# Optimization experiments

Measured on AMD Instinct MI355X. Metric: run time of the kernel, lower is better.

Reference implementation:

```python
import jax, jax.numpy as jnp
import numpy as np

# static multi-scale pyramid (must match spatial_shapes array in setup_inputs)
SPATIAL = ((100, 100), (50, 50), (25, 25), (13, 13))
E, H, L, P = 256, 8, 4, 8   # embed_dims, num_heads, num_levels, num_points
BS, NQ = 2, 10000
LEN_VAL = sum(h * w for h, w in SPATIAL)


def _bilinear_gather(val, grid, Hs, Ws):
    """val: [BH, Hs*Ws, d]; grid: [BH, N, 2] in [-1,1].
    Matches F.grid_sample(mode='bilinear', padding_mode='zeros', align_corners=False)."""
    x = (grid[..., 0] + 1.0) * (Ws * 0.5) - 0.5
    y = (grid[..., 1] + 1.0) * (Hs * 0.5) - 0.5
    x0 = jnp.floor(x).astype(jnp.int32)
    y0 = jnp.floor(y).astype(jnp.int32)
    x1, y1 = x0 + 1, y0 + 1
    wx1 = x - x0.astype(x.dtype)
    wy1 = y - y0.astype(y.dtype)
    wx0, wy0 = 1.0 - wx1, 1.0 - wy1

    def corner(xi, yi, w):
        valid = (xi >= 0) & (xi < Ws) & (yi >= 0) & (yi < Hs)
        idx = jnp.clip(yi, 0, Hs - 1) * Ws + jnp.clip(xi, 0, Ws - 1)  # [BH, N]
        v = jnp.take_along_axis(val, idx[..., None], axis=1)          # [BH, N, d]
        return v * (w * valid.astype(w.dtype))[..., None]

    return (corner(x0, y0, wx0 * wy0) + corner(x1, y0, wx1 * wy0)
            + corner(x0, y1, wx0 * wy1) + corner(x1, y1, wx1 * wy1))


def setup_inputs() -> dict:
    key = jax.random.key(0)
    ks = jax.random.split(key, 10)
    scale = 1.0 / np.sqrt(E)
    inp = {
        'query': jax.random.normal(ks[0], (BS, NQ, E), jnp.float32),
        'value': jax.random.normal(ks[1], (BS, LEN_VAL, E), jnp.float32),
        'query_pos': 0.1 * jax.random.normal(ks[2], (BS, NQ, E), jnp.float32),
        'reference_points': jax.random.uniform(ks[3], (BS, NQ, L, 2), jnp.float32),
        'spatial_shapes': jnp.array(SPATIAL, dtype=jnp.int32),
        'W_off': 0.02 * jax.random.normal(ks[4], (E, H * L * P * 2), jnp.float32),
        'b_off': 0.5 * jax.random.normal(ks[5], (H * L * P * 2,), jnp.float32),
        'W_attn': 0.02 * jax.random.normal(ks[6], (E, H * L * P), jnp.float32),
        'b_attn': jnp.zeros((H * L * P,), jnp.float32),
        'W_val': scale * jax.random.normal(ks[7], (E, E), jnp.float32),
        'b_val': jnp.zeros((E,), jnp.float32),
        'W_out': scale * jax.random.normal(ks[8], (E, E), jnp.float32),
        'b_out': jnp.zeros((E,), jnp.float32),
    }
    return inp


def reference(query, value, query_pos, reference_points, spatial_shapes,
              W_off, b_off, W_attn, b_attn, W_val, b_val, W_out, b_out):
    d = E // H
    q = query + query_pos                                        # [bs, nq, E]
    bs, nq, _ = q.shape
    v = (value @ W_val + b_val).reshape(bs, LEN_VAL, H, d)       # [bs, len, H, d]
    off = (q @ W_off + b_off).reshape(bs, nq, H, L, P, 2)
    aw = jax.nn.softmax((q @ W_attn + b_attn).reshape(bs, nq, H, L * P), axis=-1)
    aw = aw.reshape(bs, nq, H, L, P)
    # normalizer is (W, H) per level
    norm = jnp.stack([spatial_shapes[:, 1], spatial_shapes[:, 0]], -1).astype(q.dtype)
    loc = reference_points[:, :, None, :, None, :] + off / norm[None, None, None, :, None, :]
    grids = 2.0 * loc - 1.0                                      # [bs, nq, H, L, P, 2]

    out = jnp.zeros((bs, nq, H, d), q.dtype)
    start = 0
    for lvl, (Hs, Ws) in enumerate(SPATIAL):
        v_l = v[:, start:start + Hs * Ws]                        # [bs, HW, H, d]
        start += Hs * Ws
        v_l = v_l.transpose(0, 2, 1, 3).reshape(bs * H, Hs * Ws, d)
        g_l = grids[:, :, :, lvl].transpose(0, 2, 1, 3, 4).reshape(bs * H, nq * P, 2)
        s = _bilinear_gather(v_l, g_l, Hs, Ws).reshape(bs, H, nq, P, d)
        w_l = aw[:, :, :, lvl].transpose(0, 2, 1, 3)             # [bs, H, nq, P]
        out = out + jnp.einsum('bhnpc,bhnp->bnhc', s, w_l)
    return out.reshape(bs, nq, E) @ W_out + b_out
```

## Files before the change

kernel.cpp:

```cpp
#include <hip/hip_runtime.h>


#define EE   256
#define HH   8
#define LL   4
#define NQq  10000
#define BSB  2
#define LENV 13294
#define MQ   16
#define ROWS_V (BSB * LENV)

#define VWS_OFF 393216

typedef unsigned short u16;
typedef unsigned int   u32;
typedef __attribute__((ext_vector_type(8))) short bf16x8;
typedef __attribute__((ext_vector_type(4))) float f32x4;

__device__ __forceinline__ u32 bf16_of(float f) {
  u32 u = __float_as_uint(f);
  return (u + 0x7FFFu + ((u >> 16) & 1u)) >> 16;
}
__device__ __forceinline__ float blo(u32 u) { return __uint_as_float(u << 16); }
__device__ __forceinline__ float bhi(u32 u) { return __uint_as_float(u & 0xFFFF0000u); }

__device__ __forceinline__ uint4 pack8(const float* f) {
  uint4 u;
  u.x = bf16_of(f[0]) | (bf16_of(f[1]) << 16);
  u.y = bf16_of(f[2]) | (bf16_of(f[3]) << 16);
  u.z = bf16_of(f[4]) | (bf16_of(f[5]) << 16);
  u.w = bf16_of(f[6]) | (bf16_of(f[7]) << 16);
  return u;
}

__device__ __forceinline__ void acc8(float o[8], uint4 q, float w) {
  o[0] += w * blo(q.x); o[1] += w * bhi(q.x);
  o[2] += w * blo(q.y); o[3] += w * bhi(q.y);
  o[4] += w * blo(q.z); o[5] += w * bhi(q.z);
  o[6] += w * blo(q.w); o[7] += w * bhi(q.w);
}

__global__ __launch_bounds__(64) void k_prep(
    const float* __restrict__ W_off, const float* __restrict__ W_attn,
    const float* __restrict__ W_val, const float* __restrict__ W_out,
    u16* __restrict__ wcat, u16* __restrict__ wval, u16* __restrict__ wout) {
  const int tile = blockIdx.x >> 3, s = blockIdx.x & 7;
  const int l = threadIdx.x, quad = l >> 4, r16 = l & 15;
  float f[8];
  u16* dst;
  if (tile < 48) {
    int col = tile * 16 + r16;
#pragma unroll
    for (int j = 0; j < 8; ++j) {
      int k = s * 32 + quad * 8 + j;
      f[j] = (col < 512) ? W_off[k * 512 + col] : W_attn[k * 256 + (col - 512)];
    }
    dst = wcat + ((tile * 8 + s) * 64 + l) * 8;
  } else if (tile < 64) {
    int col = (tile - 48) * 16 + r16;
#pragma unroll
    for (int j = 0; j < 8; ++j) f[j] = W_val[(s * 32 + quad * 8 + j) * 256 + col];
    dst = wval + (((tile - 48) * 8 + s) * 64 + l) * 8;
  } else {
    int col = (tile - 64) * 16 + r16;
#pragma unroll
    for (int j = 0; j < 8; ++j) f[j] = W_out[(s * 32 + quad * 8 + j) * 256 + col];
    dst = wout + (((tile - 64) * 8 + s) * 64 + l) * 8;
  }
  *(uint4*)dst = pack8(f);
}

__global__ __launch_bounds__(512) void k_valproj(
    const float* __restrict__ value, const float* __restrict__ b_val,
    const u16* __restrict__ wval, u16* __restrict__ v_ws) {
  __shared__ __align__(16) u16 sA[64][264];
  const int tid = threadIdx.x;
  const int g0 = blockIdx.x * 64;
#pragma unroll
  for (int ch = 0; ch < 4; ++ch) {
    int fidx = ch * 4096 + tid * 8;
    int row = fidx >> 8, col = fidx & 255;
    int g = g0 + row;
    float fv[8] = {0.f, 0.f, 0.f, 0.f, 0.f, 0.f, 0.f, 0.f};
    if (g < ROWS_V) {
      float4 a = *(const float4*)(value + (long)g * 256 + col);
      float4 b = *(const float4*)(value + (long)g * 256 + col + 4);
      fv[0] = a.x; fv[1] = a.y; fv[2] = a.z; fv[3] = a.w;
      fv[4] = b.x; fv[5] = b.y; fv[6] = b.z; fv[7] = b.w;
    }
    *(uint4*)&sA[row][col] = pack8(fv);
  }
  __syncthreads();
  const int wave = tid >> 6, lane = tid & 63, quad = lane >> 4, r16 = lane & 15;
  f32x4 acc[2][4] = {};
  for (int s = 0; s < 8; ++s) {
    bf16x8 af[4];
#pragma unroll
    for (int mt = 0; mt < 4; ++mt)
      af[mt] = *(const bf16x8*)&sA[mt * 16 + r16][s * 32 + quad * 8];
#pragma unroll
    for (int nt = 0; nt < 2; ++nt) {
      int ntg = wave * 2 + nt;
      bf16x8 bfg = *(const bf16x8*)(wval + ((ntg * 8 + s) * 64 + lane) * 8);
#pragma unroll
      for (int mt = 0; mt < 4; ++mt)
        acc[nt][mt] = __builtin_amdgcn_mfma_f32_16x16x32_bf16(af[mt], bfg, acc[nt][mt], 0, 0, 0);
    }
  }
  __syncthreads();
#pragma unroll
  for (int nt = 0; nt < 2; ++nt) {
    int col = (wave * 2 + nt) * 16 + r16;
    float bias = b_val[col];
#pragma unroll
    for (int mt = 0; mt < 4; ++mt)
#pragma unroll
      for (int rr = 0; rr < 4; ++rr)
        sA[mt * 16 + quad * 4 + rr][col] = (u16)bf16_of(acc[nt][mt][rr] + bias);
  }
  __syncthreads();
#pragma unroll
  for (int it = 0; it < 4; ++it) {
    int chunk = it * 512 + tid;
    int r  = chunk >> 5;
    int hc = chunk & 31;
    int h2 = hc >> 2, qq = hc & 3;
    int g = g0 + r;
    if (g < ROWS_V) {
      int bb = g / LENV, pix = g - bb * LENV;
      *(uint4*)(v_ws + ((long)((bb * 8 + h2) * LENV + pix) * 32 + qq * 8)) =
          *(const uint4*)&sA[r][h2 * 32 + qq * 8];
    }
  }
}

__global__ __launch_bounds__(512, 6) void k_attn(
    const float* __restrict__ query, const float* __restrict__ query_pos,
    const float* __restrict__ refpts,
    const float* __restrict__ b_off, const float* __restrict__ b_attn,
    const float* __restrict__ b_out,
    const u16* __restrict__ wcat, const u16* __restrict__ wout,
    const char* __restrict__ wsb, float* __restrict__ out) {
  __shared__ __align__(16) char smem[49408];
  u16   (*sQ)[264]   = (u16(*)[264])smem;
  float (*sC)[772]   = (float(*)[772])smem;
  uint2 (*sWgt)[256] = (uint2(*)[256])smem;
  u32   (*sOff)[256] = (u32(*)[256])(smem + 32768);
  u16   (*sO)[264]   = (u16(*)[264])smem;

  const int tid = threadIdx.x;
  const int g0 = blockIdx.x * MQ;
  const int b = g0 / NQq;
  const int q0 = g0 - b * NQq;
  const int wave = tid >> 6, lane = tid & 63, quad = lane >> 4, r16 = lane & 15;

  {
    int fidx = tid * 8;
    int row = fidx >> 8, col = fidx & 255;
    long base = ((long)(b * NQq + q0 + row)) * 256 + col;
    float4 a0 = *(const float4*)(query + base);
    float4 a1 = *(const float4*)(query + base + 4);
    float4 p0 = *(const float4*)(query_pos + base);
    float4 p1 = *(const float4*)(query_pos + base + 4);
    float fv[8] = {a0.x + p0.x, a0.y + p0.y, a0.z + p0.z, a0.w + p0.w,
                   a1.x + p1.x, a1.y + p1.y, a1.z + p1.z, a1.w + p1.w};
    *(uint4*)&sQ[row][col] = pack8(fv);
  }
  __syncthreads();

  f32x4 acc[6] = {};
  for (int s = 0; s < 8; ++s) {
    bf16x8 af = *(const bf16x8*)&sQ[r16][s * 32 + quad * 8];
#pragma unroll
    for (int t6 = 0; t6 < 6; ++t6) {
      int tile = wave * 6 + t6;
      bf16x8 bfg = *(const bf16x8*)(wcat + ((tile * 8 + s) * 64 + lane) * 8);
      acc[t6] = __builtin_amdgcn_mfma_f32_16x16x32_bf16(af, bfg, acc[t6], 0, 0, 0);
    }
  }
  __syncthreads();
#pragma unroll
  for (int t6 = 0; t6 < 6; ++t6) {
    int col = (wave * 6 + t6) * 16 + r16;
#pragma unroll
    for (int rr = 0; rr < 4; ++rr)
      sC[quad * 4 + rr][col] = acc[t6][rr];
  }
  __syncthreads();

  {
    const int m = tid >> 5, hh = (tid >> 2) & 7, g = tid & 3;
    float* p = &sC[m][512 + hh * 32 + g * 8];
    const float* ba = b_attn + hh * 32 + g * 8;
    float v[8];
    float mx = -1e30f;
#pragma unroll
    for (int j = 0; j < 8; ++j) { v[j] = p[j] + ba[j]; mx = fmaxf(mx, v[j]); }
    mx = fmaxf(mx, __shfl_xor(mx, 1));
    mx = fmaxf(mx, __shfl_xor(mx, 2));
    float sum = 0.f;
#pragma unroll
    for (int j = 0; j < 8; ++j) { v[j] = __expf(v[j] - mx); sum += v[j]; }
    sum += __shfl_xor(sum, 1);
    sum += __shfl_xor(sum, 2);
    float inv = 1.f / sum;
#pragma unroll
    for (int j = 0; j < 8; ++j) p[j] = v[j] * inv;
  }
  __syncthreads();

  uint2 wrecs[8];
  u32   orecs[8];
  {
    const int s = tid & 255, mh = tid >> 8;
    const int l = (s >> 3) & 3;
    const int WlI[4] = {100, 50, 25, 13};
    const int baseI[4] = {0, 10000, 12500, 13125};
    const int Wl = WlI[l], Hl = WlI[l], base = baseI[l];
    const float WlF = (float)Wl;
    const float box = b_off[2 * s], boy = b_off[2 * s + 1];
#pragma unroll
    for (int mm = 0; mm < 8; ++mm) {
      int m = mh * 8 + mm;
      float w = sC[m][512 + s];
      float ax = sC[m][2 * s], ay = sC[m][2 * s + 1];
      float2 rp = *(const float2*)(refpts + (((long)(b * NQq + q0 + m)) * LL + l) * 2);
      float x = rp.x * WlF + (ax + box) - 0.5f;
      float y = rp.y * WlF + (ay + boy) - 0.5f;
      float fx0 = floorf(x), fy0 = floorf(y);
      int x0 = (int)fx0, y0 = (int)fy0;
      float fx = x - fx0, fy = y - fy0;
      bool xv0 = (x0 >= 0) & (x0 < Wl);
      bool xv1 = (x0 >= -1) & (x0 < Wl - 1);
      bool yv0 = (y0 >= 0) & (y0 < Hl);
      bool yv1 = (y0 >= -1) & (y0 < Hl - 1);
      float w00 = w * (1.f - fx) * (1.f - fy) * (float)(xv0 & yv0);
      float w01 = w * fx * (1.f - fy) * (float)(xv1 & yv0);
      float w10 = w * (1.f - fx) * fy * (float)(xv0 & yv1);
      float w11 = w * fx * fy * (float)(xv1 & yv1);
      int x0a = min(max(x0, -1), Wl - 1);
      int y0a = min(max(y0, -1), Hl - 1);
      int y1c = min(max(y0 + 1, 0), Hl - 1);
      int o00u = base + y0a * Wl + x0a;
      u32 dyu  = (u32)((y1c - y0a) * Wl);
      wrecs[mm].x = bf16_of(w00) | (bf16_of(w01) << 16);
      wrecs[mm].y = bf16_of(w10) | (bf16_of(w11) << 16);
      orecs[mm]   = (u32)(o00u + 128) | (dyu << 14);
    }
  }
  __syncthreads();
  {
    const int s = tid & 255, mh = tid >> 8;
    const int jsw = (s & 224) | ((s + (s >> 5)) & 31);
#pragma unroll
    for (int mm = 0; mm < 8; ++mm) {
      sWgt[mh * 8 + mm][jsw] = wrecs[mm];
      sOff[mh * 8 + mm][jsw] = orecs[mm];
    }
  }
  __syncthreads();

  {
    const int c4 = tid & 3, hh = (tid >> 2) & 7, m = tid >> 5;
    const u32 vbm = (u32)VWS_OFF + (u32)(b * 8 + hh) * (u32)(LENV * 64)
                  + (u32)c4 * 16u - 8192u;
    float oacc[8] = {};
#pragma unroll
    for (int i = 0; i < 32; i += 2) {
      const int sr0 = (hh << 5) | ((i + hh) & 31);
      const int sr1 = (hh << 5) | ((i + 1 + hh) & 31);
      uint2 wr0 = sWgt[m][sr0];
      uint2 wr1 = sWgt[m][sr1];
      u32 po0 = sOff[m][sr0];
      u32 po1 = sOff[m][sr1];
      u32 oa0 = vbm + ((po0 & 0x3FFFu) << 6);
      u32 oa1 = oa0 + ((po0 >> 14) << 6);
      u32 ob0 = vbm + ((po1 & 0x3FFFu) << 6);
      u32 ob1 = ob0 + ((po1 >> 14) << 6);
      uint4 qa00 = *(const uint4*)(wsb + oa0);
      uint4 qa01 = *(const uint4*)(wsb + oa0 + 64);
      uint4 qa10 = *(const uint4*)(wsb + oa1);
      uint4 qa11 = *(const uint4*)(wsb + oa1 + 64);
      uint4 qb00 = *(const uint4*)(wsb + ob0);
      uint4 qb01 = *(const uint4*)(wsb + ob0 + 64);
      uint4 qb10 = *(const uint4*)(wsb + ob1);
      uint4 qb11 = *(const uint4*)(wsb + ob1 + 64);
      __builtin_amdgcn_sched_barrier(0);
      acc8(oacc, qa00, blo(wr0.x));
      acc8(oacc, qa01, bhi(wr0.x));
      acc8(oacc, qa10, blo(wr0.y));
      acc8(oacc, qa11, bhi(wr0.y));
      acc8(oacc, qb00, blo(wr1.x));
      acc8(oacc, qb01, bhi(wr1.x));
      acc8(oacc, qb10, blo(wr1.y));
      acc8(oacc, qb11, bhi(wr1.y));
    }
    __syncthreads();
    *(uint4*)&sO[m][hh * 32 + c4 * 8] = pack8(oacc);
  }
  __syncthreads();

  f32x4 acc2[2] = {};
  for (int s = 0; s < 8; ++s) {
    bf16x8 af = *(const bf16x8*)&sO[r16][s * 32 + quad * 8];
#pragma unroll
    for (int t2 = 0; t2 < 2; ++t2) {
      int tile = wave * 2 + t2;
      bf16x8 bfg = *(const bf16x8*)(wout + ((tile * 8 + s) * 64 + lane) * 8);
      acc2[t2] = __builtin_amdgcn_mfma_f32_16x16x32_bf16(af, bfg, acc2[t2], 0, 0, 0);
    }
  }
#pragma unroll
  for (int t2 = 0; t2 < 2; ++t2) {
    int col = (wave * 2 + t2) * 16 + r16;
    float bias = b_out[col];
#pragma unroll
    for (int rr = 0; rr < 4; ++rr) {
      int row = quad * 4 + rr;
      out[((long)(b * NQq + q0 + row)) * 256 + col] = acc2[t2][rr] + bias;
    }
  }
}

extern "C" void kernel_launch(void* const* d_in, const int* in_sizes, int n_in,
                              void* d_out, int out_size, void* d_ws, size_t ws_size,
                              hipStream_t stream) {
  const float* query     = (const float*)d_in[0];
  const float* value     = (const float*)d_in[1];
  const float* query_pos = (const float*)d_in[2];
  const float* refpts    = (const float*)d_in[3];
  const float* W_off     = (const float*)d_in[5];
  const float* b_off     = (const float*)d_in[6];
  const float* W_attn    = (const float*)d_in[7];
  const float* b_attn    = (const float*)d_in[8];
  const float* W_val     = (const float*)d_in[9];
  const float* b_val     = (const float*)d_in[10];
  const float* W_out     = (const float*)d_in[11];
  const float* b_out     = (const float*)d_in[12];
  float* out = (float*)d_out;

  char* ws = (char*)d_ws;
  u16* wcat = (u16*)ws;
  u16* v_ws = (u16*)(ws + VWS_OFF);
  u16* wval = (u16*)(ws + VWS_OFF + 13613056);
  u16* wout = (u16*)(ws + VWS_OFF + 13613056 + 131072);

  k_prep<<<dim3(80 * 8), dim3(64), 0, stream>>>(W_off, W_attn, W_val, W_out,
                                                wcat, wval, wout);
  k_valproj<<<dim3((ROWS_V + 63) / 64), dim3(512), 0, stream>>>(value, b_val, wval, v_ws);
  k_attn<<<dim3(BSB * NQq / MQ), dim3(512), 0, stream>>>(
      query, query_pos, refpts, b_off, b_attn, b_out, wcat, wout, ws, out);
}
```

Baseline: 236.6 us.

## Remap sampling threads to split x-corners across lanes and handle two queries each

The bilinear sampling stage now assigns 8 lanes per (query, head) group. Each lane pair splits the left and right x-corners, and each thread accumulates two queries (m0 and m0+8) instead of one. Partial sums are combined with a cross-lane shuffle, and only half the lanes write the result. The shared-memory swizzle is changed to depend on the query row, to match the new read pattern. The aim is better memory-level parallelism and a different gather coalescing pattern, at the cost of extra shuffles and half-idle stores.

```diff
diff --git a/kernel.cpp b/kernel.cpp
--- a/kernel.cpp
+++ b/kernel.cpp
@@ -251,52 +251,59 @@
   __syncthreads();
   {
     const int s = tid & 255, mh = tid >> 8;
-    const int jsw = (s & 224) | ((s + (s >> 5)) & 31);
 #pragma unroll
     for (int mm = 0; mm < 8; ++mm) {
-      sWgt[mh * 8 + mm][jsw] = wrecs[mm];
-      sOff[mh * 8 + mm][jsw] = orecs[mm];
-    }
-  }
-  __syncthreads();
-
-  {
-    const int c4 = tid & 3, hh = (tid >> 2) & 7, m = tid >> 5;
+      int m = mh * 8 + mm;
+      int col = (s & 224) | ((s + m) & 31);
+      sWgt[m][col] = wrecs[mm];
+      sOff[m][col] = orecs[mm];
+    }
+  }
+  __syncthreads();
+
+  {
+    const int c8 = tid & 7, g8 = tid >> 3;
+    const int m0 = g8 & 7, hh = g8 >> 3;
+    const int xsel = c8 >> 2;
+    const int sb = hh << 5;
     const u32 vbm = (u32)VWS_OFF + (u32)(b * 8 + hh) * (u32)(LENV * 64)
-                  + (u32)c4 * 16u - 8192u;
-    float oacc[8] = {};
-#pragma unroll
-    for (int i = 0; i < 32; i += 2) {
-      const int sr0 = (hh << 5) | ((i + hh) & 31);
-      const int sr1 = (hh << 5) | ((i + 1 + hh) & 31);
-      uint2 wr0 = sWgt[m][sr0];
-      uint2 wr1 = sWgt[m][sr1];
-      u32 po0 = sOff[m][sr0];
-      u32 po1 = sOff[m][sr1];
-      u32 oa0 = vbm + ((po0 & 0x3FFFu) << 6);
-      u32 oa1 = oa0 + ((po0 >> 14) << 6);
-      u32 ob0 = vbm + ((po1 & 0x3FFFu) << 6);
-      u32 ob1 = ob0 + ((po1 >> 14) << 6);
-      uint4 qa00 = *(const uint4*)(wsb + oa0);
-      uint4 qa01 = *(const uint4*)(wsb + oa0 + 64);
-      uint4 qa10 = *(const uint4*)(wsb + oa1);
-      uint4 qa11 = *(const uint4*)(wsb + oa1 + 64);
-      uint4 qb00 = *(const uint4*)(wsb + ob0);
-      uint4 qb01 = *(const uint4*)(wsb + ob0 + 64);
-      uint4 qb10 = *(const uint4*)(wsb + ob1);
-      uint4 qb11 = *(const uint4*)(wsb + ob1 + 64);
-      __builtin_amdgcn_sched_barrier(0);
-      acc8(oacc, qa00, blo(wr0.x));
-      acc8(oacc, qa01, bhi(wr0.x));
-      acc8(oacc, qa10, blo(wr0.y));
-      acc8(oacc, qa11, bhi(wr0.y));
-      acc8(oacc, qb00, blo(wr1.x));
-      acc8(oacc, qb01, bhi(wr1.x));
-      acc8(oacc, qb10, blo(wr1.y));
-      acc8(oacc, qb11, bhi(wr1.y));
+                  + (u32)(c8 & 3) * 16u + (u32)xsel * 64u - 8192u;
+    float oa[8] = {}, ob[8] = {};
+#pragma unroll 4
+    for (int i = 0; i < 32; ++i) {
+      const int colA = sb | ((i + m0) & 31);
+      const int colB = sb | ((i + m0 + 8) & 31);
+      uint2 wrA = sWgt[m0][colA];
+      u32   poA = sOff[m0][colA];
+      uint2 wrB = sWgt[m0 + 8][colB];
+      u32   poB = sOff[m0 + 8][colB];
+      u32 a0 = vbm + ((poA & 0x3FFFu) << 6);
+      u32 a1 = a0 + ((poA >> 14) << 6);
+      u32 b0 = vbm + ((poB & 0x3FFFu) << 6);
+      u32 b1 = b0 + ((poB >> 14) << 6);
+      uint4 qa0 = *(const uint4*)(wsb + a0);
+      uint4 qa1 = *(const uint4*)(wsb + a1);
+      uint4 qb0 = *(const uint4*)(wsb + b0);
+      uint4 qb1 = *(const uint4*)(wsb + b1);
+      float wA0 = xsel ? bhi(wrA.x) : blo(wrA.x);
+      float wA1 = xsel ? bhi(wrA.y) : blo(wrA.y);
+      float wB0 = xsel ? bhi(wrB.x) : blo(wrB.x);
+      float wB1 = xsel ? bhi(wrB.y) : blo(wrB.y);
+      acc8(oa, qa0, wA0);
+      acc8(oa, qa1, wA1);
+      acc8(ob, qb0, wB0);
+      acc8(ob, qb1, wB1);
+    }
+#pragma unroll
+    for (int j = 0; j < 8; ++j) {
+      oa[j] += __shfl_xor(oa[j], 4);
+      ob[j] += __shfl_xor(ob[j], 4);
     }
     __syncthreads();
-    *(uint4*)&sO[m][hh * 32 + c4 * 8] = pack8(oacc);
+    if (!xsel) {
+      *(uint4*)&sO[m0][hh * 32 + c8 * 8]     = pack8(oa);
+      *(uint4*)&sO[m0 + 8][hh * 32 + c8 * 8] = pack8(ob);
+    }
   }
   __syncthreads();
 
```

Result: faster. 228.9 us (median of 2 runs) (-3.3%).
